# Kernel tuning notes

Hardware: AMD Instinct MI355X
Metric: run time of the kernel (lower is better)

## Reference

```python
import jax, jax.numpy as jnp
import numpy as np

PI = np.pi


def setup_inputs() -> dict:
    key = jax.random.key(0)
    ks = jax.random.split(key, 20)
    B, L, D = 2, 1024, 512
    TP = 16      # n_sets(4) * planes_per_set(4)
    PP = 16      # pos_planes
    MAXL = 8192
    sc = 1.0 / np.sqrt(D)
    return {
        "x": jax.random.normal(ks[0], (B, L, D), jnp.float32),
        "Wk": jax.random.normal(ks[1], (TP, D), jnp.float32) * sc,
        "bk": jnp.zeros((TP,), jnp.float32),
        "Wq": jax.random.normal(ks[2], (TP, D), jnp.float32) * sc,
        "bq": jnp.zeros((TP,), jnp.float32),
        "Wv": jax.random.normal(ks[3], (D, D), jnp.float32) * sc,
        "bv": jnp.zeros((D,), jnp.float32),
        "ln_g": jnp.ones((D,), jnp.float32),
        "ln_b": jnp.zeros((D,), jnp.float32),
        "Wo": jax.random.normal(ks[4], (D, D), jnp.float32) * sc,
        "bo": jnp.zeros((D,), jnp.float32),
        "set_w": jnp.ones((4,), jnp.float32),
        "pos_phases": jax.random.normal(ks[5], (MAXL, PP), jnp.float32) * PI,
        "pos_weight": jnp.ones((1,), jnp.float32),
        "Wg1": jax.random.normal(ks[6], (D // 2, D), jnp.float32) * sc,
        "bg1": jnp.zeros((D // 2,), jnp.float32),
        "Wg2": jax.random.normal(ks[7], (1, D // 2), jnp.float32) * np.sqrt(2.0 / D),
        "bg2": jnp.zeros((1,), jnp.float32),
    }


def reference(x, Wk, bk, Wq, bq, Wv, bv, ln_g, ln_b, Wo, bo,
              set_w, pos_phases, pos_weight, Wg1, bg1, Wg2, bg2):
    B, L, D = x.shape
    n_sets, pps = 4, 4

    # --- content phasor memory ---
    kp = jnp.tanh(x @ Wk.T + bk) * PI                       # [B,L,16]
    qp = jnp.tanh(x @ Wq.T + bq) * PI
    key_ph = jnp.exp(1j * kp).reshape(B, L, n_sets, pps)    # [B,L,S,P] c64
    qry_ph = jnp.exp(1j * qp).reshape(B, L, n_sets, pps)
    Vr = x @ Wv.T + bv                                       # [B,L,D]
    V = Vr.astype(jnp.complex64)

    bound = key_ph[..., None] * V[:, :, None, None, :]       # [B,L,S,P,D] c64
    mem = jnp.cumsum(bound, axis=1)                          # prefix-sum memory
    retr = (mem * jnp.conj(qry_ph)[..., None]).sum(axis=3).real   # [B,L,S,D]
    w = jax.nn.softmax(set_w)
    content = (retr * w[None, None, :, None]).sum(axis=2)    # [B,L,D]

    # --- positional cos/sin memory ---
    ph = pos_phases[:L]                                      # [L,PP]
    c = jnp.cos(ph)[None]                                    # [1,L,PP]
    s = jnp.sin(ph)[None]
    br = Vr[:, :, None, :] * c[..., None]                    # [B,L,PP,D]
    bi = Vr[:, :, None, :] * s[..., None]
    mr = jnp.cumsum(br, axis=1)
    mi = jnp.cumsum(bi, axis=1)
    pos = (mr * c[..., None] + mi * s[..., None]).sum(axis=2)  # [B,L,D]

    # --- gate, mix, normalize, output proj ---
    g = jax.nn.sigmoid(
        jax.nn.gelu(x @ Wg1.T + bg1, approximate=False) @ Wg2.T + bg2)  # [B,L,1]
    total = g * content + (1.0 - g) * jax.nn.sigmoid(pos_weight) * pos
    norm = jnp.sqrt(jnp.arange(1, L + 1, dtype=x.dtype) * pps)[None, :, None]
    t = total / norm
    mu = t.mean(-1, keepdims=True)
    var = ((t - mu) ** 2).mean(-1, keepdims=True)
    tn = (t - mu) / jnp.sqrt(var + 1e-5) * ln_g + ln_b
    return x + tn @ Wo.T + bo
```

## Files before the change

### kernel.cpp

```cpp
#include <hip/hip_runtime.h>
#include <math.h>

#define PI_F 3.14159265358979323846f
#define BB 2
#define LL 1024
#define NCH 64
#define CHUNK 32
#define NCHUNK (LL/CHUNK)
#define NW 1408
#define YH 384

typedef __attribute__((ext_vector_type(8))) short short8;
typedef __attribute__((ext_vector_type(4))) float floatx4;
typedef const __attribute__((address_space(1))) unsigned int cgu32;
typedef __attribute__((address_space(3))) unsigned int lu32;

__device__ __forceinline__ unsigned short f2bf(float f){
    unsigned u = __float_as_uint(f);
    unsigned r = (u + 0x7fff + ((u >> 16) & 1)) >> 16;
    return (unsigned short)r;
}

__global__ __launch_bounds__(128) void k_prep(
    const float* __restrict__ Wv, const float* __restrict__ Wg1,
    const float* __restrict__ Wk, const float* __restrict__ Wq,
    const float* __restrict__ Wo,
    const float* __restrict__ bv, const float* __restrict__ bg1,
    const float* __restrict__ bk, const float* __restrict__ bq,
    const float* __restrict__ bo, const float* __restrict__ x,
    unsigned short* __restrict__ Wb, float* __restrict__ bcat,
    unsigned short* __restrict__ xb)
{
    const int bid = blockIdx.x, tid = threadIdx.x;
    if (bid < NW){
        const int n = bid;
        const float* src = (n<512) ? Wv  + (size_t)n*512
                         : (n<768) ? Wg1 + (size_t)(n-512)*512
                         : (n<784) ? Wk  + (size_t)(n-768)*512
                         : (n<800) ? Wq  + (size_t)(n-784)*512
                         : (n<896) ? (const float*)0
                                   : Wo  + (size_t)(n-896)*512;
        float4 v = make_float4(0.f,0.f,0.f,0.f);
        if (src) v = ((const float4*)src)[tid];
        ushort4 o; o.x=f2bf(v.x); o.y=f2bf(v.y); o.z=f2bf(v.z); o.w=f2bf(v.w);
        ((ushort4*)(Wb + (size_t)n*512))[tid] = o;
        if (tid == 0)
            bcat[n] = (n<512)?bv[n] : (n<768)?bg1[n-512] : (n<784)?bk[n-768]
                    : (n<800)?bq[n-784] : (n<896)?0.f : bo[n-896];
    } else {
        const size_t i = (size_t)(bid - NW)*128 + tid;
        float4 v = ((const float4*)x)[i];
        ushort4 o; o.x=f2bf(v.x); o.y=f2bf(v.y); o.z=f2bf(v.z); o.w=f2bf(v.w);
        ((ushort4*)xb)[i] = o;
    }
}

__device__ __forceinline__ void gemm64x64(
    const unsigned short* Ag, const unsigned short* Bg,
    short* As, short* Bs, int tid, floatx4 acc[2][2])
{
    const int lane = tid & 63, w = tid >> 6;
    const int wm = w & 1, wn = w >> 1;
    const int q = lane >> 4, m15 = lane & 15;
    for (int kt = 0; kt < 512; kt += 64) {
        __syncthreads();
        #pragma unroll
        for (int i = 0; i < 2; ++i) {
            const int rowbase = (w*2 + i) * 8;
            const int r  = rowbase + (lane >> 3);
            const int gb = (lane & 7) ^ (r & 7);
            const unsigned short* ga  = Ag + (size_t)r*512 + kt + gb*8;
            const unsigned short* gbp = Bg + (size_t)r*512 + kt + gb*8;
            __builtin_amdgcn_global_load_lds((cgu32*)(const void*)ga,
                                             (lu32*)(As + rowbase*64), 16, 0, 0);
            __builtin_amdgcn_global_load_lds((cgu32*)(const void*)gbp,
                                             (lu32*)(Bs + rowbase*64), 16, 0, 0);
        }
        __syncthreads();
        #pragma unroll
        for (int k32 = 0; k32 < 64; k32 += 32) {
            short8 af[2], bf[2];
            #pragma unroll
            for (int t = 0; t < 2; ++t) {
                const int ra  = 32*wm + 16*t + m15;
                const int sba = ((k32>>3) + q) ^ (ra & 7);
                af[t] = *(const short8*)(As + ra*64 + sba*8);
                const int rb  = 32*wn + 16*t + m15;
                const int sbb = ((k32>>3) + q) ^ (rb & 7);
                bf[t] = *(const short8*)(Bs + rb*64 + sbb*8);
            }
            #pragma unroll
            for (int mt = 0; mt < 2; ++mt)
                #pragma unroll
                for (int nt = 0; nt < 2; ++nt)
                    acc[mt][nt] = __builtin_amdgcn_mfma_f32_16x16x32_bf16(
                        af[mt], bf[nt], acc[mt][nt], 0, 0, 0);
        }
    }
}

__global__ __launch_bounds__(256) void kg1(
    const unsigned short* __restrict__ xb, const unsigned short* __restrict__ Wb,
    const float* __restrict__ bcat, unsigned short* __restrict__ Vt,
    float* __restrict__ Yh)
{
    __shared__ short As[64*64], Bs[64*64];
    const int tid = threadIdx.x;
    const int row0 = blockIdx.x*64, n0 = blockIdx.y*64;
    floatx4 acc[2][2];
    #pragma unroll
    for (int mt=0;mt<2;++mt)
        #pragma unroll
        for (int nt=0;nt<2;++nt) acc[mt][nt] = (floatx4){0.f,0.f,0.f,0.f};
    gemm64x64(xb + (size_t)row0*512, Wb + (size_t)n0*512, As, Bs, tid, acc);
    const int lane = tid & 63, w = tid >> 6;
    const int wm = w & 1, wn = w >> 1, q = lane >> 4, m15 = lane & 15;
    if (n0 < 512){
        const int b = row0 >> 10, lb = row0 & 1023;
        #pragma unroll
        for (int mt=0;mt<2;++mt)
            #pragma unroll
            for (int nt=0;nt<2;++nt){
                const int d = n0 + 32*wn + 16*nt + m15;
                const float bb = bcat[d];
                const int l0 = lb + 32*wm + 16*mt + q*4;
                ushort4 o;
                o.x = f2bf(acc[mt][nt][0] + bb);
                o.y = f2bf(acc[mt][nt][1] + bb);
                o.z = f2bf(acc[mt][nt][2] + bb);
                o.w = f2bf(acc[mt][nt][3] + bb);
                *(ushort4*)(Vt + ((size_t)(b*512 + d))*1024 + l0) = o;
            }
    } else {
        #pragma unroll
        for (int mt=0;mt<2;++mt)
            #pragma unroll
            for (int nt=0;nt<2;++nt){
                const int n = n0 + 32*wn + 16*nt + m15;
                const float bb = bcat[n];
                #pragma unroll
                for (int reg=0;reg<4;++reg){
                    const int m = row0 + 32*wm + 16*mt + q*4 + reg;
                    Yh[(size_t)m*YH + (n-512)] = acc[mt][nt][reg] + bb;
                }
            }
    }
}

__global__ __launch_bounds__(256) void k_act(
    const float* __restrict__ Yh, const float* __restrict__ Wg2,
    const float* __restrict__ bg2, const float* __restrict__ set_w,
    const float* __restrict__ pos_phases, const float* __restrict__ pos_weight,
    unsigned short* __restrict__ ab, unsigned short* __restrict__ Rb,
    unsigned short* __restrict__ aT)
{
    const int tid = threadIdx.x, lane = tid & 63, w = tid >> 6;
    const int row0 = blockIdx.x * 8;
    float s0=set_w[0], s1=set_w[1], s2=set_w[2], s3=set_w[3];
    float m = fmaxf(fmaxf(s0,s1), fmaxf(s2,s3));
    float e0=expf(s0-m), e1=expf(s1-m), e2=expf(s2-m), e3=expf(s3-m);
    float esum = e0+e1+e2+e3;
    float spw = 1.f/(1.f+expf(-pos_weight[0]));
    float b2 = bg2[0];
    #pragma unroll
    for (int rr=0;rr<2;++rr){
        int row = row0 + w + 4*rr;
        const float* yrow = Yh + (size_t)row*YH;
        float hs = 0.f;
        #pragma unroll
        for (int i=0;i<4;++i){
            float hv = yrow[lane + 64*i];
            float ge = 0.5f*hv*(1.f + erff(hv*0.70710678118f));
            hs += ge * Wg2[lane + 64*i];
        }
        #pragma unroll
        for (int off=32; off; off>>=1) hs += __shfl_xor(hs, off, 64);
        float g = 1.f/(1.f+expf(-(hs + b2)));
        if (lane < 16){
            int j = lane;
            int l = row & (LL-1);
            int b = row >> 10;
            float kang = PI_F*tanhf(yrow[256 + j]);
            float qang = PI_F*tanhf(yrow[272 + j]);
            float wsm = (j<4?e0: j<8?e1: j<12?e2: e3) / esum;
            float rnorm = 1.f/(2.f*sqrtf((float)(l+1)));
            float av[4], rv[4];
            av[0] = cosf(kang); av[1] = sinf(kang);
            float cw = g*wsm*rnorm;
            rv[0] = cw*cosf(qang); rv[1] = cw*sinf(qang);
            float ph = pos_phases[(size_t)l*16 + j];
            float pc = cosf(ph), ps = sinf(ph);
            av[2] = pc; av[3] = ps;
            float cp = (1.f-g)*spw*rnorm;
            rv[2] = cp*pc; rv[3] = cp*ps;
            unsigned short* arow = ab + (size_t)row*NCH;
            unsigned short* Rrow = Rb + (size_t)row*NCH;
            #pragma unroll
            for (int t=0;t<4;++t){
                arow[16*t + j] = f2bf(av[t]);
                Rrow[16*t + j] = f2bf(rv[t]);
                aT[((size_t)b*NCH + 16*t + j)*1024 + l] = f2bf(av[t]);
            }
        }
    }
}

__global__ __launch_bounds__(256) void k2a_chunksum(
    const unsigned short* __restrict__ aT, const unsigned short* __restrict__ Vt,
    float* __restrict__ P)
{
    const int c = blockIdx.x, b = blockIdx.y, z = blockIdx.z;
    const int tid = threadIdx.x, lane = tid & 63, w = tid >> 6;
    const int q = lane >> 4, m15 = lane & 15;
    short8 af[4];
    #pragma unroll
    for (int mt=0;mt<4;++mt)
        af[mt] = *(const short8*)(aT + ((size_t)b*NCH + 16*mt + m15)*1024 + c*32 + q*8);
    floatx4 acc[4][4];
    #pragma unroll
    for (int mt=0;mt<4;++mt)
        #pragma unroll
        for (int nt=0;nt<4;++nt) acc[mt][nt] = (floatx4){0.f,0.f,0.f,0.f};
    #pragma unroll
    for (int nt=0;nt<4;++nt){
        const int d = z*256 + w*64 + 16*nt + m15;
        short8 bf = *(const short8*)(Vt + ((size_t)(b*512 + d))*1024 + c*32 + q*8);
        #pragma unroll
        for (int mt=0;mt<4;++mt)
            acc[mt][nt] = __builtin_amdgcn_mfma_f32_16x16x32_bf16(af[mt], bf, acc[mt][nt], 0,0,0);
    }
    float* Pc = P + ((size_t)(b*NCHUNK + c))*512*NCH;
    #pragma unroll
    for (int mt=0;mt<4;++mt)
        #pragma unroll
        for (int nt=0;nt<4;++nt){
            const int d = z*256 + w*64 + 16*nt + m15;
            const int ch0 = 16*mt + q*4;
            *(floatx4*)(Pc + (size_t)d*NCH + ch0) = acc[mt][nt];
        }
}

__global__ __launch_bounds__(256) void k2b_prefix(
    const float* __restrict__ P, unsigned short* __restrict__ S0t)
{
    const int b = blockIdx.y;
    const size_t idx = (size_t)blockIdx.x*256 + threadIdx.x;
    float run = 0.f;
    for (int c=0;c<NCHUNK;++c){
        const size_t o = ((size_t)(b*NCHUNK + c))*512*NCH + idx;
        float v = P[o];
        S0t[o] = f2bf(run);
        run += v;
    }
}

__global__ __launch_bounds__(256) void k2c_scan(
    const unsigned short* __restrict__ ab, const unsigned short* __restrict__ Rb,
    const unsigned short* __restrict__ Vt, const unsigned short* __restrict__ S0t,
    const float* __restrict__ ln_g, const float* __restrict__ ln_b,
    unsigned short* __restrict__ Tn)
{
    __shared__ short Msh[32*32];
    __shared__ float Tsh[32*512];
    const int c = blockIdx.x, b = blockIdx.y;
    const int tid = threadIdx.x, lane = tid & 63, w = tid >> 6;
    const int q = lane >> 4, m15 = lane & 15;
    const int grow = b*1024 + c*32;

    if (w == 0){
        floatx4 mcc[2][2];
        #pragma unroll
        for (int mt=0;mt<2;++mt)
            #pragma unroll
            for (int nt=0;nt<2;++nt) mcc[mt][nt] = (floatx4){0.f,0.f,0.f,0.f};
        #pragma unroll
        for (int ks=0;ks<2;++ks){
            short8 ra[2], bb[2];
            #pragma unroll
            for (int t=0;t<2;++t){
                ra[t] = *(const short8*)(Rb + (size_t)(grow + 16*t + m15)*NCH + ks*32 + q*8);
                bb[t] = *(const short8*)(ab + (size_t)(grow + 16*t + m15)*NCH + ks*32 + q*8);
            }
            #pragma unroll
            for (int mt=0;mt<2;++mt)
                #pragma unroll
                for (int nt=0;nt<2;++nt)
                    mcc[mt][nt] = __builtin_amdgcn_mfma_f32_16x16x32_bf16(
                        ra[mt], bb[nt], mcc[mt][nt], 0,0,0);
        }
        #pragma unroll
        for (int mt=0;mt<2;++mt)
            #pragma unroll
            for (int nt=0;nt<2;++nt){
                const int nl = 16*nt + m15;
                #pragma unroll
                for (int reg=0;reg<4;++reg){
                    const int ml = 16*mt + q*4 + reg;
                    Msh[ml*32 + nl] = (nl <= ml) ? (short)f2bf(mcc[mt][nt][reg]) : (short)0;
                }
            }
    }
    __syncthreads();

    short8 a1[2], a2[2][2];
    #pragma unroll
    for (int mt=0;mt<2;++mt){
        a1[mt] = *(const short8*)(Msh + (16*mt + m15)*32 + q*8);
        #pragma unroll
        for (int ks=0;ks<2;++ks)
            a2[ks][mt] = *(const short8*)(Rb + (size_t)(grow + 16*mt + m15)*NCH + ks*32 + q*8);
    }
    floatx4 acc[2][8];
    #pragma unroll
    for (int mt=0;mt<2;++mt)
        #pragma unroll
        for (int nt=0;nt<8;++nt) acc[mt][nt] = (floatx4){0.f,0.f,0.f,0.f};
    const unsigned short* S0c = S0t + ((size_t)(b*NCHUNK + c))*512*NCH;
    #pragma unroll
    for (int nt=0;nt<8;++nt){
        const int d = w*128 + 16*nt + m15;
        short8 b1 = *(const short8*)(Vt + ((size_t)(b*512 + d))*1024 + c*32 + q*8);
        #pragma unroll
        for (int mt=0;mt<2;++mt)
            acc[mt][nt] = __builtin_amdgcn_mfma_f32_16x16x32_bf16(a1[mt], b1, acc[mt][nt], 0,0,0);
        #pragma unroll
        for (int ks=0;ks<2;++ks){
            short8 b2 = *(const short8*)(S0c + (size_t)d*NCH + ks*32 + q*8);
            #pragma unroll
            for (int mt=0;mt<2;++mt)
                acc[mt][nt] = __builtin_amdgcn_mfma_f32_16x16x32_bf16(a2[ks][mt], b2, acc[mt][nt], 0,0,0);
        }
    }
    #pragma unroll
    for (int mt=0;mt<2;++mt)
        #pragma unroll
        for (int nt=0;nt<8;++nt){
            const int d = w*128 + 16*nt + m15;
            #pragma unroll
            for (int reg=0;reg<4;++reg)
                Tsh[(16*mt + q*4 + reg)*512 + d] = acc[mt][nt][reg];
        }
    __syncthreads();

    #pragma unroll
    for (int i=0;i<8;++i){
        const int r = w*8 + i;
        float s=0.f, sq=0.f;
        #pragma unroll
        for (int t=0;t<8;++t){
            float v = Tsh[r*512 + lane + 64*t];
            s += v; sq += v*v;
        }
        #pragma unroll
        for (int off=32; off; off>>=1){
            s += __shfl_xor(s, off, 64); sq += __shfl_xor(sq, off, 64);
        }
        float mu  = s*(1.f/512.f);
        float var = sq*(1.f/512.f) - mu*mu;
        float rsd = rsqrtf(var + 1e-5f);
        unsigned short* trow = Tn + (size_t)(grow + r)*512;
        #pragma unroll
        for (int t=0;t<8;++t){
            const int d = lane + 64*t;
            float v = (Tsh[r*512 + d] - mu)*rsd*ln_g[d] + ln_b[d];
            trow[d] = f2bf(v);
        }
    }
}

__global__ __launch_bounds__(256) void kg2(
    const unsigned short* __restrict__ Tn, const unsigned short* __restrict__ Wb,
    const float* __restrict__ bcat, const float* __restrict__ x,
    float* __restrict__ out)
{
    __shared__ short As[64*64], Bs[64*64];
    const int tid = threadIdx.x;
    const int row0 = blockIdx.x*64, n0 = blockIdx.y*64;
    floatx4 acc[2][2];
    #pragma unroll
    for (int mt=0;mt<2;++mt)
        #pragma unroll
        for (int nt=0;nt<2;++nt) acc[mt][nt] = (floatx4){0.f,0.f,0.f,0.f};
    gemm64x64(Tn + (size_t)row0*512, Wb + (size_t)(896+n0)*512, As, Bs, tid, acc);
    const int lane = tid & 63, w = tid >> 6;
    const int wm = w & 1, wn = w >> 1, q = lane >> 4, m15 = lane & 15;
    #pragma unroll
    for (int mt=0;mt<2;++mt)
        #pragma unroll
        for (int nt=0;nt<2;++nt){
            const int n = n0 + 32*wn + 16*nt + m15;
            const float bb = bcat[896 + n];
            #pragma unroll
            for (int reg=0;reg<4;++reg){
                const int m = row0 + 32*wm + 16*mt + q*4 + reg;
                out[(size_t)m*512 + n] = x[(size_t)m*512 + n] + acc[mt][nt][reg] + bb;
            }
        }
}

extern "C" void kernel_launch(void* const* d_in, const int* in_sizes, int n_in,
                              void* d_out, int out_size, void* d_ws, size_t ws_size,
                              hipStream_t stream) {
    const float* x    = (const float*)d_in[0];
    const float* Wk   = (const float*)d_in[1];
    const float* bk   = (const float*)d_in[2];
    const float* Wq   = (const float*)d_in[3];
    const float* bq   = (const float*)d_in[4];
    const float* Wv   = (const float*)d_in[5];
    const float* bv   = (const float*)d_in[6];
    const float* ln_g = (const float*)d_in[7];
    const float* ln_b = (const float*)d_in[8];
    const float* Wo   = (const float*)d_in[9];
    const float* bo   = (const float*)d_in[10];
    const float* set_w      = (const float*)d_in[11];
    const float* pos_phases = (const float*)d_in[12];
    const float* pos_weight = (const float*)d_in[13];
    const float* Wg1  = (const float*)d_in[14];
    const float* bg1  = (const float*)d_in[15];
    const float* Wg2  = (const float*)d_in[16];
    const float* bg2  = (const float*)d_in[17];
    float* out = (float*)d_out;

    float* ws   = (float*)d_ws;
    float* Yh   = ws;
    float* P    = Yh + (size_t)2048*YH;
    float* bcat = P  + (size_t)BB*NCHUNK*512*NCH;
    unsigned short* Wb  = (unsigned short*)(bcat + NW);
    unsigned short* xb  = Wb  + (size_t)NW*512;
    unsigned short* Vt  = xb  + (size_t)2048*512;
    unsigned short* ab  = Vt  + (size_t)BB*512*1024;
    unsigned short* Rb  = ab  + (size_t)2048*NCH;
    unsigned short* aT  = Rb  + (size_t)2048*NCH;
    unsigned short* S0t = aT  + (size_t)BB*NCH*1024;
    unsigned short* Tn  = S0t + (size_t)BB*NCHUNK*512*NCH;

    k_prep<<<dim3(NW + 2048), 128, 0, stream>>>(
        Wv,Wg1,Wk,Wq,Wo, bv,bg1,bk,bq,bo, x, Wb, bcat, xb);
    kg1<<<dim3(2048/64, 14), 256, 0, stream>>>(xb, Wb, bcat, Vt, Yh);
    k_act<<<dim3(2048/8), 256, 0, stream>>>(
        Yh, Wg2, bg2, set_w, pos_phases, pos_weight, ab, Rb, aT);
    k2a_chunksum<<<dim3(NCHUNK, BB, 2), 256, 0, stream>>>(aT, Vt, P);
    k2b_prefix<<<dim3(512*NCH/256, BB), 256, 0, stream>>>(P, S0t);
    k2c_scan<<<dim3(NCHUNK, BB), 256, 0, stream>>>(ab, Rb, Vt, S0t, ln_g, ln_b, Tn);
    kg2<<<dim3(2048/64, 512/64), 256, 0, stream>>>(Tn, Wb, bcat, x, out);
}
```

Baseline: 135.2 us.

## Fuse chunked scan into one sequential kernel and fold LayerNorm into output GEMM

Replaces the three-kernel chunk-sum / prefix / intra-chunk scan pipeline with a single kernel. Each block owns a 64-wide slice of D and walks all chunks in order, carrying the running state in registers and staging it in LDS as bf16. This removes the fp32 P and bf16 S0t intermediates and two launches. LayerNorm is moved into the output GEMM, which reads the fp32 T directly, computes row statistics and normalizes while building the A tile. The cost is very low parallelism in the scan (only 16 blocks running a serial chunk loop) and statistics that are recomputed redundantly in every N-block of the GEMM.

```diff
diff --git a/kernel.cpp b/kernel.cpp
--- a/kernel.cpp
+++ b/kernel.cpp
@@ -12,6 +12,7 @@
 
 typedef __attribute__((ext_vector_type(8))) short short8;
 typedef __attribute__((ext_vector_type(4))) float floatx4;
+typedef __attribute__((ext_vector_type(2))) unsigned int uint2v;
 typedef const __attribute__((address_space(1))) unsigned int cgu32;
 typedef __attribute__((address_space(3))) unsigned int lu32;
 
@@ -60,7 +61,6 @@
     short* As, short* Bs, int tid, floatx4 acc[2][2])
 {
     const int lane = tid & 63, w = tid >> 6;
-    const int wm = w & 1, wn = w >> 1;
     const int q = lane >> 4, m15 = lane & 15;
     for (int kt = 0; kt < 512; kt += 64) {
         __syncthreads();
@@ -82,10 +82,10 @@
             short8 af[2], bf[2];
             #pragma unroll
             for (int t = 0; t < 2; ++t) {
-                const int ra  = 32*wm + 16*t + m15;
+                const int ra  = 32*(w & 1) + 16*t + m15;
                 const int sba = ((k32>>3) + q) ^ (ra & 7);
                 af[t] = *(const short8*)(As + ra*64 + sba*8);
-                const int rb  = 32*wn + 16*t + m15;
+                const int rb  = 32*(w >> 1) + 16*t + m15;
                 const int sbb = ((k32>>3) + q) ^ (rb & 7);
                 bf[t] = *(const short8*)(Bs + rb*64 + sbb*8);
             }
@@ -205,185 +205,207 @@
     }
 }
 
-__global__ __launch_bounds__(256) void k2a_chunksum(
+__global__ __launch_bounds__(256) void k_scan(
+    const unsigned short* __restrict__ ab, const unsigned short* __restrict__ Rb,
     const unsigned short* __restrict__ aT, const unsigned short* __restrict__ Vt,
-    float* __restrict__ P)
-{
-    const int c = blockIdx.x, b = blockIdx.y, z = blockIdx.z;
+    float* __restrict__ T)
+{
+    __shared__ short Msh[32*32];
+    __shared__ short Ssh[64*64];
+    const int b = blockIdx.y, d0 = blockIdx.x*64;
     const int tid = threadIdx.x, lane = tid & 63, w = tid >> 6;
     const int q = lane >> 4, m15 = lane & 15;
-    short8 af[4];
+    const int dw = w*16 + m15;
+    const int d  = d0 + dw;
+
+    floatx4 S[4];
     #pragma unroll
-    for (int mt=0;mt<4;++mt)
-        af[mt] = *(const short8*)(aT + ((size_t)b*NCH + 16*mt + m15)*1024 + c*32 + q*8);
-    floatx4 acc[4][4];
-    #pragma unroll
-    for (int mt=0;mt<4;++mt)
-        #pragma unroll
-        for (int nt=0;nt<4;++nt) acc[mt][nt] = (floatx4){0.f,0.f,0.f,0.f};
-    #pragma unroll
-    for (int nt=0;nt<4;++nt){
-        const int d = z*256 + w*64 + 16*nt + m15;
-        short8 bf = *(const short8*)(Vt + ((size_t)(b*512 + d))*1024 + c*32 + q*8);
+    for (int mt=0;mt<4;++mt) S[mt] = (floatx4){0.f,0.f,0.f,0.f};
+
+    for (int c = 0; c < NCHUNK; ++c){
+        const int grow = b*1024 + c*32;
+        #pragma unroll
+        for (int mt=0;mt<4;++mt){
+            unsigned p0 = (unsigned)f2bf(S[mt][0]) | ((unsigned)f2bf(S[mt][1])<<16);
+            unsigned p1 = (unsigned)f2bf(S[mt][2]) | ((unsigned)f2bf(S[mt][3])<<16);
+            const int gw = 2*mt + (q>>1);
+            const int adr = dw*64 + ((gw ^ (m15&7))<<3) + ((q&1)<<2);
+            *(uint2v*)(Ssh + adr) = (uint2v){p0, p1};
+        }
+        if (w == 0){
+            short8 ra[2][2], ba[2][2];
+            #pragma unroll
+            for (int ks=0;ks<2;++ks)
+                #pragma unroll
+                for (int t=0;t<2;++t){
+                    ra[ks][t] = *(const short8*)(Rb + (size_t)(grow + 16*t + m15)*NCH + ks*32 + q*8);
+                    ba[ks][t] = *(const short8*)(ab + (size_t)(grow + 16*t + m15)*NCH + ks*32 + q*8);
+                }
+            floatx4 mcc[2][2];
+            #pragma unroll
+            for (int mt=0;mt<2;++mt)
+                #pragma unroll
+                for (int nt=0;nt<2;++nt) mcc[mt][nt] = (floatx4){0.f,0.f,0.f,0.f};
+            #pragma unroll
+            for (int ks=0;ks<2;++ks)
+                #pragma unroll
+                for (int mt=0;mt<2;++mt)
+                    #pragma unroll
+                    for (int nt=0;nt<2;++nt)
+                        mcc[mt][nt] = __builtin_amdgcn_mfma_f32_16x16x32_bf16(
+                            ra[ks][mt], ba[ks][nt], mcc[mt][nt], 0,0,0);
+            #pragma unroll
+            for (int mt=0;mt<2;++mt)
+                #pragma unroll
+                for (int nt=0;nt<2;++nt){
+                    const int nl = 16*nt + m15;
+                    #pragma unroll
+                    for (int reg=0;reg<4;++reg){
+                        const int ml = 16*mt + q*4 + reg;
+                        Msh[ml*32 + nl] = (nl <= ml) ? (short)f2bf(mcc[mt][nt][reg]) : (short)0;
+                    }
+                }
+        }
+        __syncthreads();
+
+        short8 a1[2];
+        #pragma unroll
+        for (int mt=0;mt<2;++mt)
+            a1[mt] = *(const short8*)(Msh + (16*mt + m15)*32 + q*8);
+        short8 s0[2];
+        #pragma unroll
+        for (int ks=0;ks<2;++ks){
+            const int gr = 4*ks + q;
+            s0[ks] = *(const short8*)(Ssh + dw*64 + ((gr ^ (m15&7))<<3));
+        }
+        short8 vf = *(const short8*)(Vt + ((size_t)(b*512 + d))*1024 + c*32 + q*8);
+        short8 rA[2][2];
+        #pragma unroll
+        for (int ks=0;ks<2;++ks)
+            #pragma unroll
+            for (int mt=0;mt<2;++mt)
+                rA[ks][mt] = *(const short8*)(Rb + (size_t)(grow + 16*mt + m15)*NCH + ks*32 + q*8);
+        short8 aA[4];
         #pragma unroll
         for (int mt=0;mt<4;++mt)
-            acc[mt][nt] = __builtin_amdgcn_mfma_f32_16x16x32_bf16(af[mt], bf, acc[mt][nt], 0,0,0);
-    }
-    float* Pc = P + ((size_t)(b*NCHUNK + c))*512*NCH;
-    #pragma unroll
-    for (int mt=0;mt<4;++mt)
-        #pragma unroll
-        for (int nt=0;nt<4;++nt){
-            const int d = z*256 + w*64 + 16*nt + m15;
-            const int ch0 = 16*mt + q*4;
-            *(floatx4*)(Pc + (size_t)d*NCH + ch0) = acc[mt][nt];
-        }
-}
-
-__global__ __launch_bounds__(256) void k2b_prefix(
-    const float* __restrict__ P, unsigned short* __restrict__ S0t)
-{
-    const int b = blockIdx.y;
-    const size_t idx = (size_t)blockIdx.x*256 + threadIdx.x;
-    float run = 0.f;
-    for (int c=0;c<NCHUNK;++c){
-        const size_t o = ((size_t)(b*NCHUNK + c))*512*NCH + idx;
-        float v = P[o];
-        S0t[o] = f2bf(run);
-        run += v;
-    }
-}
-
-__global__ __launch_bounds__(256) void k2c_scan(
-    const unsigned short* __restrict__ ab, const unsigned short* __restrict__ Rb,
-    const unsigned short* __restrict__ Vt, const unsigned short* __restrict__ S0t,
-    const float* __restrict__ ln_g, const float* __restrict__ ln_b,
-    unsigned short* __restrict__ Tn)
-{
-    __shared__ short Msh[32*32];
-    __shared__ float Tsh[32*512];
-    const int c = blockIdx.x, b = blockIdx.y;
+            aA[mt] = *(const short8*)(aT + ((size_t)(b*NCH + 16*mt + m15))*1024 + c*32 + q*8);
+
+        floatx4 t2[2];
+        #pragma unroll
+        for (int mt=0;mt<2;++mt){
+            t2[mt] = (floatx4){0.f,0.f,0.f,0.f};
+            t2[mt] = __builtin_amdgcn_mfma_f32_16x16x32_bf16(a1[mt],    vf,    t2[mt], 0,0,0);
+            t2[mt] = __builtin_amdgcn_mfma_f32_16x16x32_bf16(rA[0][mt], s0[0], t2[mt], 0,0,0);
+            t2[mt] = __builtin_amdgcn_mfma_f32_16x16x32_bf16(rA[1][mt], s0[1], t2[mt], 0,0,0);
+        }
+        #pragma unroll
+        for (int mt=0;mt<4;++mt)
+            S[mt] = __builtin_amdgcn_mfma_f32_16x16x32_bf16(aA[mt], vf, S[mt], 0,0,0);
+
+        #pragma unroll
+        for (int mt=0;mt<2;++mt)
+            #pragma unroll
+            for (int reg=0;reg<4;++reg)
+                T[(size_t)(grow + 16*mt + q*4 + reg)*512 + d] = t2[mt][reg];
+        __syncthreads();
+    }
+}
+
+__global__ __launch_bounds__(256) void kg2ln(
+    const float* __restrict__ T, const unsigned short* __restrict__ Wb,
+    const float* __restrict__ bcat, const float* __restrict__ ln_g,
+    const float* __restrict__ ln_b, const float* __restrict__ x,
+    float* __restrict__ out)
+{
+    __shared__ short As[64*64], Bs[64*64];
+    __shared__ float muL[64], rsL[64];
     const int tid = threadIdx.x, lane = tid & 63, w = tid >> 6;
     const int q = lane >> 4, m15 = lane & 15;
-    const int grow = b*1024 + c*32;
-
-    if (w == 0){
-        floatx4 mcc[2][2];
-        #pragma unroll
-        for (int mt=0;mt<2;++mt)
-            #pragma unroll
-            for (int nt=0;nt<2;++nt) mcc[mt][nt] = (floatx4){0.f,0.f,0.f,0.f};
-        #pragma unroll
-        for (int ks=0;ks<2;++ks){
-            short8 ra[2], bb[2];
-            #pragma unroll
-            for (int t=0;t<2;++t){
-                ra[t] = *(const short8*)(Rb + (size_t)(grow + 16*t + m15)*NCH + ks*32 + q*8);
-                bb[t] = *(const short8*)(ab + (size_t)(grow + 16*t + m15)*NCH + ks*32 + q*8);
-            }
-            #pragma unroll
-            for (int mt=0;mt<2;++mt)
-                #pragma unroll
-                for (int nt=0;nt<2;++nt)
-                    mcc[mt][nt] = __builtin_amdgcn_mfma_f32_16x16x32_bf16(
-                        ra[mt], bb[nt], mcc[mt][nt], 0,0,0);
-        }
-        #pragma unroll
-        for (int mt=0;mt<2;++mt)
-            #pragma unroll
-            for (int nt=0;nt<2;++nt){
-                const int nl = 16*nt + m15;
-                #pragma unroll
-                for (int reg=0;reg<4;++reg){
-                    const int ml = 16*mt + q*4 + reg;
-                    Msh[ml*32 + nl] = (nl <= ml) ? (short)f2bf(mcc[mt][nt][reg]) : (short)0;
-                }
-            }
-    }
-    __syncthreads();
-
-    short8 a1[2], a2[2][2];
-    #pragma unroll
-    for (int mt=0;mt<2;++mt){
-        a1[mt] = *(const short8*)(Msh + (16*mt + m15)*32 + q*8);
-        #pragma unroll
-        for (int ks=0;ks<2;++ks)
-            a2[ks][mt] = *(const short8*)(Rb + (size_t)(grow + 16*mt + m15)*NCH + ks*32 + q*8);
-    }
-    floatx4 acc[2][8];
-    #pragma unroll
-    for (int mt=0;mt<2;++mt)
-        #pragma unroll
-        for (int nt=0;nt<8;++nt) acc[mt][nt] = (floatx4){0.f,0.f,0.f,0.f};
-    const unsigned short* S0c = S0t + ((size_t)(b*NCHUNK + c))*512*NCH;
-    #pragma unroll
-    for (int nt=0;nt<8;++nt){
-        const int d = w*128 + 16*nt + m15;
-        short8 b1 = *(const short8*)(Vt + ((size_t)(b*512 + d))*1024 + c*32 + q*8);
-        #pragma unroll
-        for (int mt=0;mt<2;++mt)
-            acc[mt][nt] = __builtin_amdgcn_mfma_f32_16x16x32_bf16(a1[mt], b1, acc[mt][nt], 0,0,0);
-        #pragma unroll
-        for (int ks=0;ks<2;++ks){
-            short8 b2 = *(const short8*)(S0c + (size_t)d*NCH + ks*32 + q*8);
-            #pragma unroll
-            for (int mt=0;mt<2;++mt)
-                acc[mt][nt] = __builtin_amdgcn_mfma_f32_16x16x32_bf16(a2[ks][mt], b2, acc[mt][nt], 0,0,0);
-        }
-    }
-    #pragma unroll
-    for (int mt=0;mt<2;++mt)
-        #pragma unroll
-        for (int nt=0;nt<8;++nt){
-            const int d = w*128 + 16*nt + m15;
-            #pragma unroll
-            for (int reg=0;reg<4;++reg)
-                Tsh[(16*mt + q*4 + reg)*512 + d] = acc[mt][nt][reg];
-        }
-    __syncthreads();
-
-    #pragma unroll
-    for (int i=0;i<8;++i){
-        const int r = w*8 + i;
+    const int row0 = blockIdx.x*64, n0 = blockIdx.y*64;
+
+    for (int i=0;i<16;++i){
+        const int r = w*16 + i;
+        const float* tr = T + (size_t)(row0 + r)*512;
         float s=0.f, sq=0.f;
         #pragma unroll
         for (int t=0;t<8;++t){
-            float v = Tsh[r*512 + lane + 64*t];
+            float v = tr[lane + 64*t];
             s += v; sq += v*v;
         }
         #pragma unroll
         for (int off=32; off; off>>=1){
             s += __shfl_xor(s, off, 64); sq += __shfl_xor(sq, off, 64);
         }
-        float mu  = s*(1.f/512.f);
-        float var = sq*(1.f/512.f) - mu*mu;
-        float rsd = rsqrtf(var + 1e-5f);
-        unsigned short* trow = Tn + (size_t)(grow + r)*512;
-        #pragma unroll
-        for (int t=0;t<8;++t){
-            const int d = lane + 64*t;
-            float v = (Tsh[r*512 + d] - mu)*rsd*ln_g[d] + ln_b[d];
-            trow[d] = f2bf(v);
-        }
-    }
-}
-
-__global__ __launch_bounds__(256) void kg2(
-    const unsigned short* __restrict__ Tn, const unsigned short* __restrict__ Wb,
-    const float* __restrict__ bcat, const float* __restrict__ x,
-    float* __restrict__ out)
-{
-    __shared__ short As[64*64], Bs[64*64];
-    const int tid = threadIdx.x;
-    const int row0 = blockIdx.x*64, n0 = blockIdx.y*64;
+        if (lane == 0){
+            float mu = s*(1.f/512.f);
+            float var = sq*(1.f/512.f) - mu*mu;
+            muL[r] = mu; rsL[r] = rsqrtf(var + 1e-5f);
+        }
+    }
+    __syncthreads();
+
     floatx4 acc[2][2];
     #pragma unroll
     for (int mt=0;mt<2;++mt)
         #pragma unroll
         for (int nt=0;nt<2;++nt) acc[mt][nt] = (floatx4){0.f,0.f,0.f,0.f};
-    gemm64x64(Tn + (size_t)row0*512, Wb + (size_t)(896+n0)*512, As, Bs, tid, acc);
-    const int lane = tid & 63, w = tid >> 6;
-    const int wm = w & 1, wn = w >> 1, q = lane >> 4, m15 = lane & 15;
+
+    const unsigned short* Bg = Wb + (size_t)(896 + n0)*512;
+    for (int kt = 0; kt < 512; kt += 64) {
+        __syncthreads();
+        short8 av[2];
+        #pragma unroll
+        for (int i = 0; i < 2; ++i) {
+            const int rowbase = (w*2 + i) * 8;
+            const int r  = rowbase + (lane >> 3);
+            const int gb = (lane & 7) ^ (r & 7);
+            __builtin_amdgcn_global_load_lds(
+                (cgu32*)(const void*)(Bg + (size_t)r*512 + kt + gb*8),
+                (lu32*)(Bs + rowbase*64), 16, 0, 0);
+            const float* tp = T + (size_t)(row0 + r)*512 + kt + gb*8;
+            float4 t0 = *(const float4*)tp;
+            float4 t1 = *(const float4*)(tp + 4);
+            const float* gp = ln_g + kt + gb*8;
+            const float* bp = ln_b + kt + gb*8;
+            float4 g0 = *(const float4*)gp, g1 = *(const float4*)(gp + 4);
+            float4 b0 = *(const float4*)bp, b1 = *(const float4*)(bp + 4);
+            const float mu = muL[r], rs = rsL[r];
+            short8 o;
+            o[0] = (short)f2bf((t0.x - mu)*rs*g0.x + b0.x);
+            o[1] = (short)f2bf((t0.y - mu)*rs*g0.y + b0.y);
+            o[2] = (short)f2bf((t0.z - mu)*rs*g0.z + b0.z);
+            o[3] = (short)f2bf((t0.w - mu)*rs*g0.w + b0.w);
+            o[4] = (short)f2bf((t1.x - mu)*rs*g1.x + b1.x);
+            o[5] = (short)f2bf((t1.y - mu)*rs*g1.y + b1.y);
+            o[6] = (short)f2bf((t1.z - mu)*rs*g1.z + b1.z);
+            o[7] = (short)f2bf((t1.w - mu)*rs*g1.w + b1.w);
+            av[i] = o;
+        }
+        #pragma unroll
+        for (int i = 0; i < 2; ++i)
+            *(short8*)(As + ((w*2 + i)*8)*64 + lane*8) = av[i];
+        __syncthreads();
+        #pragma unroll
+        for (int k32 = 0; k32 < 64; k32 += 32) {
+            short8 af[2], bf[2];
+            #pragma unroll
+            for (int t = 0; t < 2; ++t) {
+                const int ra  = 32*(w & 1) + 16*t + m15;
+                const int sba = ((k32>>3) + q) ^ (ra & 7);
+                af[t] = *(const short8*)(As + ra*64 + sba*8);
+                const int rb  = 32*(w >> 1) + 16*t + m15;
+                const int sbb = ((k32>>3) + q) ^ (rb & 7);
+                bf[t] = *(const short8*)(Bs + rb*64 + sbb*8);
+            }
+            #pragma unroll
+            for (int mt = 0; mt < 2; ++mt)
+                #pragma unroll
+                for (int nt = 0; nt < 2; ++nt)
+                    acc[mt][nt] = __builtin_amdgcn_mfma_f32_16x16x32_bf16(
+                        af[mt], bf[nt], acc[mt][nt], 0, 0, 0);
+        }
+    }
+    const int wm = w & 1, wn = w >> 1;
     #pragma unroll
     for (int mt=0;mt<2;++mt)
         #pragma unroll
@@ -423,24 +445,21 @@
 
     float* ws   = (float*)d_ws;
     float* Yh   = ws;
-    float* P    = Yh + (size_t)2048*YH;
-    float* bcat = P  + (size_t)BB*NCHUNK*512*NCH;
+    float* T    = Yh + (size_t)2048*YH;
+    float* bcat = T  + (size_t)2048*512;
     unsigned short* Wb  = (unsigned short*)(bcat + NW);
     unsigned short* xb  = Wb  + (size_t)NW*512;
     unsigned short* Vt  = xb  + (size_t)2048*512;
     unsigned short* ab  = Vt  + (size_t)BB*512*1024;
     unsigned short* Rb  = ab  + (size_t)2048*NCH;
     unsigned short* aT  = Rb  + (size_t)2048*NCH;
-    unsigned short* S0t = aT  + (size_t)BB*NCH*1024;
-    unsigned short* Tn  = S0t + (size_t)BB*NCHUNK*512*NCH;
 
     k_prep<<<dim3(NW + 2048), 128, 0, stream>>>(
         Wv,Wg1,Wk,Wq,Wo, bv,bg1,bk,bq,bo, x, Wb, bcat, xb);
     kg1<<<dim3(2048/64, 14), 256, 0, stream>>>(xb, Wb, bcat, Vt, Yh);
     k_act<<<dim3(2048/8), 256, 0, stream>>>(
         Yh, Wg2, bg2, set_w, pos_phases, pos_weight, ab, Rb, aT);
-    k2a_chunksum<<<dim3(NCHUNK, BB, 2), 256, 0, stream>>>(aT, Vt, P);
-    k2b_prefix<<<dim3(512*NCH/256, BB), 256, 0, stream>>>(P, S0t);
-    k2c_scan<<<dim3(NCHUNK, BB), 256, 0, stream>>>(ab, Rb, Vt, S0t, ln_g, ln_b, Tn);
-    kg2<<<dim3(2048/64, 512/64), 256, 0, stream>>>(Tn, Wb, bcat, x, out);
-}
+    k_scan<<<dim3(8, BB), 256, 0, stream>>>(ab, Rb, aT, Vt, T);
+    kg2ln<<<dim3(2048/64, 512/64), 256, 0, stream>>>(
+        T, Wb, bcat, ln_g, ln_b, x, out);
+}
```

Result: slower. 201.3 us (+48.9%).
